# Optimization experiments

Measured on AMD Instinct MI355X. Metric: run time of the kernel, lower is better.

Reference implementation:

```python
import jax, jax.numpy as jnp
import numpy as np

B, U = 64, 512            # batch, max_units
AE = 1024
UE = 256                  # unit_embedding_size
A = 256                   # target_head_attention_size


def setup_inputs() -> dict:
    key = jax.random.key(0)
    ks = jax.random.split(key, 10)
    return {
        "autoregressive_embedding": jax.random.normal(ks[0], (B, U, AE), jnp.float32),
        "own_unit_embeddings": jax.random.normal(ks[1], (B, U, UE), jnp.float32),
        "enemy_unit_embeddings": jax.random.normal(ks[2], (B, U, UE), jnp.float32),
        "nr_own_units": jax.random.randint(ks[3], (B, 1), 0, U).astype(jnp.int64),
        "nr_units_enemy": jax.random.randint(ks[4], (B, 1), 0, U).astype(jnp.int64),
        "nr_own_flags": jax.random.randint(ks[5], (B, 1), 0, 8).astype(jnp.int64),
        "Wq": jax.random.normal(ks[6], (UE + AE, A), jnp.float32) * (1.0 / np.sqrt(UE + AE)),
        "bq": jnp.zeros((A,), jnp.float32),
        "Wk": jax.random.normal(ks[7], (UE, A), jnp.float32) * (1.0 / np.sqrt(UE)),
        "bk": jnp.zeros((A,), jnp.float32),
    }


def reference(autoregressive_embedding, own_unit_embeddings, enemy_unit_embeddings,
              nr_own_units, nr_units_enemy, nr_own_flags, Wq, bq, Wk, bk):
    # combined: [B, U, AE+UE]
    combined = jnp.concatenate([autoregressive_embedding, own_unit_embeddings], axis=2)
    queries = combined @ Wq + bq                       # [B, U, A]
    keys = enemy_unit_embeddings @ Wk + bk             # [B, U, A]
    attention = jnp.einsum("bqd,bkd->bqk", queries, keys) / (A ** 0.5)  # [B, U, U]
    # Vectorized mask: rows in [nr_own_flags, nr_own_units), cols in [0, nr_units_enemy)
    idx = jnp.arange(U)
    row_ok = (idx[None, :] >= nr_own_flags) & (idx[None, :] < nr_own_units)  # [B, U]
    col_ok = idx[None, :] < nr_units_enemy                                   # [B, U]
    mask = jnp.where(row_ok[:, :, None] & col_ok[:, None, :], 1.0, 1e-9)     # [B, U, U]
    return jax.nn.softmax(attention * mask, axis=-1)
```

## Files before the change

### kernel.cpp

```cpp
#include <hip/hip_runtime.h>

constexpr int B  = 64;
constexpr int U  = 512;
constexpr int AE = 1024;
constexpr int UE = 256;
constexpr int A  = 256;
constexpr int KQ = AE + UE;

typedef _Float16 f16x8 __attribute__((ext_vector_type(8)));
typedef float    f32x4 __attribute__((ext_vector_type(4)));


__global__ void prep(const float* __restrict__ Wq, const float* __restrict__ Wk,
                     _Float16* __restrict__ BTq, _Float16* __restrict__ BTk) {
    int idx = blockIdx.x * 256 + threadIdx.x;
    const float* W;
    _Float16* Dst;
    int rem;
    if (idx < 20 * 2 * 256 * 32) { W = Wq; Dst = BTq; rem = idx; }
    else                         { W = Wk; Dst = BTk; rem = idx - 20 * 2 * 256 * 32; }
    int pos = rem & 31;
    int row = (rem >> 5) & 255;
    int kp  = rem >> 13;
    int s = pos >> 3, e = pos & 7;
    int c = ((s ^ ((row >> 1) & 3)) << 3) | e;
    int k = kp * 32 + c;
    Dst[rem] = (_Float16)W[(size_t)k * 256 + row];
}

__global__ __launch_bounds__(512) void gemm(
    const float* __restrict__ A1, int s1, int split,
    const float* __restrict__ A2, int s2,
    const _Float16* __restrict__ BT,
    const float* __restrict__ bias,
    _Float16* __restrict__ Out,
    int Ktot)
{
    __shared__ __align__(16) _Float16 Al[2][2][64][32];
    __shared__ __align__(16) _Float16 Bl[2][2][256][32];

    const int t    = threadIdx.x;
    const int lane = t & 63;
    const int w    = t >> 6;
    const int mbase = blockIdx.x * 64;

    const int wm = (w & 1) * 32;
    const int wn = (w >> 1) * 64;

    f32x4 acc[2][4] = {};

    const int ar  = t >> 3;
    const int aq  = t & 7;
    const int ap  = aq >> 2;
    const int asw = ((aq & 3) ^ ((ar >> 1) & 3)) * 8;
    const size_t grow = mbase + ar;

    float4 areg0, areg1;

    auto loadA = [&](int k0) {
        int kg = k0 + aq * 8;
        const float* src = (kg < split) ? (A1 + grow * (size_t)s1 + kg)
                                        : (A2 + grow * (size_t)s2 + (kg - split));
        areg0 = ((const float4*)src)[0];
        areg1 = ((const float4*)src)[1];
    };
    auto stageB = [&](int kb, int nb) {
        const char* g = (const char*)BT + (size_t)kb * 32768 + w * 4096 + (lane << 4);
        char* l = (char*)(&Bl[nb][0][0][0]) + w * 4096;
        #pragma unroll
        for (int i = 0; i < 4; i++)
            __builtin_amdgcn_global_load_lds(
                (const __attribute__((address_space(1))) void*)(g + i * 1024),
                (__attribute__((address_space(3))) void*)(l + i * 1024), 16, 0, 0);
    };
    auto writeA = [&](int nb) {
        f16x8 hv;
        hv[0] = (_Float16)areg0.x; hv[1] = (_Float16)areg0.y;
        hv[2] = (_Float16)areg0.z; hv[3] = (_Float16)areg0.w;
        hv[4] = (_Float16)areg1.x; hv[5] = (_Float16)areg1.y;
        hv[6] = (_Float16)areg1.z; hv[7] = (_Float16)areg1.w;
        *(f16x8*)(&Al[nb][ap][ar][asw]) = hv;
    };

    loadA(0);
    stageB(0, 0);
    writeA(0);
    asm volatile("s_waitcnt vmcnt(0) lgkmcnt(0)" ::: "memory");
    __builtin_amdgcn_s_barrier();
    __builtin_amdgcn_sched_barrier(0);

    const int rsw = (((lane & 15) >> 1) & 3);
    const int nk = Ktot >> 6;
    int cur = 0;
    for (int kb = 0; kb < nk; kb++) {
        const bool more = (kb + 1 < nk);
        if (more) {
            loadA(kb * 64 + 64);
            stageB(kb + 1, cur ^ 1);
        }
        __builtin_amdgcn_sched_barrier(0);
        #pragma unroll
        for (int p = 0; p < 2; p++) {
            f16x8 af[2], bf[4];
            #pragma unroll
            for (int mt = 0; mt < 2; mt++)
                af[mt] = *(const f16x8*)(&Al[cur][p][wm + mt * 16 + (lane & 15)][(((lane >> 4) ^ rsw)) * 8]);
            #pragma unroll
            for (int nt = 0; nt < 4; nt++)
                bf[nt] = *(const f16x8*)(&Bl[cur][p][wn + nt * 16 + (lane & 15)][(((lane >> 4) ^ rsw)) * 8]);
            #pragma unroll
            for (int mt = 0; mt < 2; mt++)
                #pragma unroll
                for (int nt = 0; nt < 4; nt++)
                    acc[mt][nt] = __builtin_amdgcn_mfma_f32_16x16x32_f16(
                        af[mt], bf[nt], acc[mt][nt], 0, 0, 0);
        }
        __builtin_amdgcn_sched_barrier(0);
        if (more) writeA(cur ^ 1);
        asm volatile("s_waitcnt vmcnt(0) lgkmcnt(0)" ::: "memory");
        __builtin_amdgcn_s_barrier();
        __builtin_amdgcn_sched_barrier(0);
        cur ^= 1;
    }

    const int col0 = wn + (lane & 15);
    const int rsub = (lane >> 4) * 4;
    #pragma unroll
    for (int nt = 0; nt < 4; nt++) {
        const int col = col0 + nt * 16;
        const float bv = bias[col];
        const int c5 = col >> 5, c31 = col & 31;
        const int sc = c31 >> 3, ei = c31 & 7;
        #pragma unroll
        for (int mt = 0; mt < 2; mt++)
            #pragma unroll
            for (int r = 0; r < 4; r++) {
                int row = mbase + wm + mt * 16 + rsub + r;
                int bb = row >> 9, u = row & 511;
                int posb = ((sc ^ ((u >> 1) & 3)) << 3) | ei;
                Out[(((size_t)bb * 8 + c5) * 512 + u) * 32 + posb] =
                    (_Float16)(acc[mt][nt][r] + bv);
            }
    }
}

__global__ __launch_bounds__(512) void attn(
    const _Float16* __restrict__ Qh, const _Float16* __restrict__ Kh,
    const int* __restrict__ nr_own_units, const int* __restrict__ nr_units_enemy,
    const int* __restrict__ nr_own_flags, float* __restrict__ Out)
{
    __shared__ __align__(16) _Float16 Ql[8][64][32];
    __shared__ __align__(16) _Float16 Kl[512][32];
    __shared__ float red[64][4];

    const int t    = threadIdx.x;
    const int lane = t & 63;
    const int w    = t >> 6;
    const int b    = blockIdx.y;
    const int qbase = blockIdx.x * 64;

    const int nf = nr_own_flags[b];
    const int nu = nr_own_units[b];
    const int ne = nr_units_enemy[b];

    const int wm = (w & 1) * 32;
    const int wn = (w >> 1) * 128;

    f16x8 qreg[4];
    {
        const _Float16* Qb = Qh + ((size_t)b * 8 * 512 + qbase) * 32;
        #pragma unroll
        for (int j = 0; j < 4; j++) {
            int s = j * 512 + t;
            int p = s >> 8, row = (s & 255) >> 2, cq = s & 3;
            qreg[j] = *(const f16x8*)(Qb + ((size_t)p * 512 + row) * 32 + cq * 8);
        }
        #pragma unroll
        for (int j = 0; j < 4; j++) {
            int s = j * 512 + t;
            int p = s >> 8, row = (s & 255) >> 2, cq = s & 3;
            *(f16x8*)(&Ql[p][row][cq * 8]) = qreg[j];
        }
    }

    const _Float16* Kb = Kh + (size_t)b * 8 * 512 * 32;
    f16x8 kreg[4];
    const int krow = t >> 2;
    const int kq   = t & 3;
    auto loadK = [&](int c) {
        const _Float16* Kc = Kb + (size_t)c * 512 * 32;
        #pragma unroll
        for (int j = 0; j < 4; j++)
            kreg[j] = *(const f16x8*)(Kc + ((size_t)(j * 128 + krow)) * 32 + kq * 8);
    };
    loadK(0);

    f32x4 acc[2][8] = {};
    const int rsw = (((lane & 15) >> 1) & 3);
    for (int c = 0; c < 8; c++) {
        __syncthreads();
        #pragma unroll
        for (int j = 0; j < 4; j++) {
            int row = j * 128 + krow;
            *(f16x8*)(&Kl[row][kq * 8]) = kreg[j];
        }
        __syncthreads();
        if (c < 7) loadK(c + 1);
        f16x8 af[2], bf[8];
        #pragma unroll
        for (int mt = 0; mt < 2; mt++)
            af[mt] = *(const f16x8*)(&Ql[c][wm + mt * 16 + (lane & 15)][((lane >> 4) ^ rsw) * 8]);
        #pragma unroll
        for (int nt = 0; nt < 8; nt++)
            bf[nt] = *(const f16x8*)(&Kl[wn + nt * 16 + (lane & 15)][((lane >> 4) ^ rsw) * 8]);
        #pragma unroll
        for (int mt = 0; mt < 2; mt++)
            #pragma unroll
            for (int nt = 0; nt < 8; nt++)
                acc[mt][nt] = __builtin_amdgcn_mfma_f32_16x16x32_f16(
                    af[mt], bf[nt], acc[mt][nt], 0, 0, 0);
    }

    const int rsub = (lane >> 4) * 4;
    #pragma unroll
    for (int mt = 0; mt < 2; mt++)
        #pragma unroll
        for (int nt = 0; nt < 8; nt++)
            #pragma unroll
            for (int r = 0; r < 4; r++) {
                int rl = wm + mt * 16 + rsub + r;
                int uq = qbase + rl;
                int col = wn + nt * 16 + (lane & 15);
                bool ok = (col < ne) && (uq >= nf) && (uq < nu);
                acc[mt][nt][r] = acc[mt][nt][r] * 0.0625f * (ok ? 1.0f : 1e-9f);
            }

    float mx[2][4];
    #pragma unroll
    for (int mt = 0; mt < 2; mt++)
        #pragma unroll
        for (int r = 0; r < 4; r++) {
            float m = acc[mt][0][r];
            #pragma unroll
            for (int nt = 1; nt < 8; nt++) m = fmaxf(m, acc[mt][nt][r]);
            #pragma unroll
            for (int off = 1; off <= 8; off <<= 1) m = fmaxf(m, __shfl_xor(m, off));
            mx[mt][r] = m;
        }
    if ((lane & 15) == 0) {
        #pragma unroll
        for (int mt = 0; mt < 2; mt++)
            #pragma unroll
            for (int r = 0; r < 4; r++)
                red[wm + mt * 16 + rsub + r][w >> 1] = mx[mt][r];
    }
    __syncthreads();
    #pragma unroll
    for (int mt = 0; mt < 2; mt++)
        #pragma unroll
        for (int r = 0; r < 4; r++) {
            f32x4 v = *(const f32x4*)(&red[wm + mt * 16 + rsub + r][0]);
            mx[mt][r] = fmaxf(fmaxf(v[0], v[1]), fmaxf(v[2], v[3]));
        }
    __syncthreads();

    float sm[2][4];
    #pragma unroll
    for (int mt = 0; mt < 2; mt++)
        #pragma unroll
        for (int r = 0; r < 4; r++) {
            float s = 0.f;
            #pragma unroll
            for (int nt = 0; nt < 8; nt++) {
                float e = __expf(acc[mt][nt][r] - mx[mt][r]);
                acc[mt][nt][r] = e;
                s += e;
            }
            #pragma unroll
            for (int off = 1; off <= 8; off <<= 1) s += __shfl_xor(s, off);
            sm[mt][r] = s;
        }
    if ((lane & 15) == 0) {
        #pragma unroll
        for (int mt = 0; mt < 2; mt++)
            #pragma unroll
            for (int r = 0; r < 4; r++)
                red[wm + mt * 16 + rsub + r][w >> 1] = sm[mt][r];
    }
    __syncthreads();

    #pragma unroll
    for (int mt = 0; mt < 2; mt++)
        #pragma unroll
        for (int r = 0; r < 4; r++) {
            int rl = wm + mt * 16 + rsub + r;
            f32x4 v = *(const f32x4*)(&red[rl][0]);
            float inv = 1.0f / (v[0] + v[1] + v[2] + v[3]);
            float* orow = Out + ((size_t)b * 512 + qbase + rl) * 512 + wn + (lane & 15);
            #pragma unroll
            for (int nt = 0; nt < 8; nt++)
                orow[nt * 16] = acc[mt][nt][r] * inv;
        }
}

extern "C" void kernel_launch(void* const* d_in, const int* in_sizes, int n_in,
                              void* d_out, int out_size, void* d_ws, size_t ws_size,
                              hipStream_t stream) {
    const float* ar    = (const float*)d_in[0];
    const float* own   = (const float*)d_in[1];
    const float* enemy = (const float*)d_in[2];
    const int*   n_own   = (const int*)d_in[3];
    const int*   n_enemy = (const int*)d_in[4];
    const int*   n_flags = (const int*)d_in[5];
    const float* Wq = (const float*)d_in[6];
    const float* bq = (const float*)d_in[7];
    const float* Wk = (const float*)d_in[8];
    const float* bk = (const float*)d_in[9];
    float* out = (float*)d_out;

    char* ws = (char*)d_ws;
    _Float16* BTq = (_Float16*)(ws);
    _Float16* BTk = (_Float16*)(ws + 655360);
    _Float16* Qh  = (_Float16*)(ws + 786432);
    _Float16* Kh  = (_Float16*)(ws + 786432 + 16777216);

    prep<<<dim3(1536), dim3(256), 0, stream>>>(Wq, Wk, BTq, BTk);

    gemm<<<dim3(512), dim3(512), 0, stream>>>(ar, AE, AE, own, UE, BTq, bq, Qh, KQ);
    gemm<<<dim3(512), dim3(512), 0, stream>>>(enemy, UE, 0, enemy, UE, BTk, bk, Kh, A);

    attn<<<dim3(8, B), dim3(512), 0, stream>>>(Qh, Kh, n_own, n_enemy, n_flags, out);
}
```

Measured before the change: 322.6 us.

## Deepen projection GEMM pipeline to four LDS stages with K=32 steps

Restructures the projection GEMM main loop from a double-buffered K=64 step into a four-stage ring of K=32 slices. B tiles are prefetched three steps ahead and A two steps ahead, and the wait uses a partial vmcnt instead of draining all loads. This aims to hide global load latency behind MFMA work. In exchange it doubles the number of barriers per K and adds clamped redundant loads at the tail, and it relies on the vmcnt(5) count being exactly right.

```diff
diff --git a/kernel.cpp b/kernel.cpp
--- a/kernel.cpp
+++ b/kernel.cpp
@@ -8,6 +8,7 @@
 constexpr int KQ = AE + UE;
 
 typedef _Float16 f16x8 __attribute__((ext_vector_type(8)));
+typedef _Float16 f16x4 __attribute__((ext_vector_type(4)));
 typedef float    f32x4 __attribute__((ext_vector_type(4)));
 
 
@@ -17,8 +18,8 @@
     const float* W;
     _Float16* Dst;
     int rem;
-    if (idx < 20 * 2 * 256 * 32) { W = Wq; Dst = BTq; rem = idx; }
-    else                         { W = Wk; Dst = BTk; rem = idx - 20 * 2 * 256 * 32; }
+    if (idx < 40 * 256 * 32) { W = Wq; Dst = BTq; rem = idx; }
+    else                     { W = Wk; Dst = BTk; rem = idx - 40 * 256 * 32; }
     int pos = rem & 31;
     int row = (rem >> 5) & 255;
     int kp  = rem >> 13;
@@ -36,11 +37,12 @@
     _Float16* __restrict__ Out,
     int Ktot)
 {
-    __shared__ __align__(16) _Float16 Al[2][2][64][32];
-    __shared__ __align__(16) _Float16 Bl[2][2][256][32];
+    __shared__ __align__(16) _Float16 Al[4][64][32];
+    __shared__ __align__(16) _Float16 Bl[4][256][32];
 
     const int t    = threadIdx.x;
     const int lane = t & 63;
+    const int l15  = lane & 15;
     const int w    = t >> 6;
     const int mbase = blockIdx.x * 64;
 
@@ -49,81 +51,87 @@
 
     f32x4 acc[2][4] = {};
 
-    const int ar  = t >> 3;
-    const int aq  = t & 7;
-    const int ap  = aq >> 2;
-    const int asw = ((aq & 3) ^ ((ar >> 1) & 3)) * 8;
+    const int ar = t >> 3;
+    const int aq = t & 7;
     const size_t grow = mbase + ar;
-
-    float4 areg0, areg1;
-
-    auto loadA = [&](int k0) {
-        int kg = k0 + aq * 8;
+    const int nk = Ktot >> 5;
+
+    auto loadA = [&](int kb, float4& dst) {
+        int kk = kb < nk ? kb : nk - 1;
+        int kg = kk * 32 + aq * 4;
         const float* src = (kg < split) ? (A1 + grow * (size_t)s1 + kg)
                                         : (A2 + grow * (size_t)s2 + (kg - split));
-        areg0 = ((const float4*)src)[0];
-        areg1 = ((const float4*)src)[1];
+        dst = *(const float4*)src;
     };
     auto stageB = [&](int kb, int nb) {
-        const char* g = (const char*)BT + (size_t)kb * 32768 + w * 4096 + (lane << 4);
-        char* l = (char*)(&Bl[nb][0][0][0]) + w * 4096;
-        #pragma unroll
-        for (int i = 0; i < 4; i++)
-            __builtin_amdgcn_global_load_lds(
-                (const __attribute__((address_space(1))) void*)(g + i * 1024),
-                (__attribute__((address_space(3))) void*)(l + i * 1024), 16, 0, 0);
-    };
-    auto writeA = [&](int nb) {
-        f16x8 hv;
-        hv[0] = (_Float16)areg0.x; hv[1] = (_Float16)areg0.y;
-        hv[2] = (_Float16)areg0.z; hv[3] = (_Float16)areg0.w;
-        hv[4] = (_Float16)areg1.x; hv[5] = (_Float16)areg1.y;
-        hv[6] = (_Float16)areg1.z; hv[7] = (_Float16)areg1.w;
-        *(f16x8*)(&Al[nb][ap][ar][asw]) = hv;
-    };
-
-    loadA(0);
+        int kk = kb < nk ? kb : nk - 1;
+        const char* g = (const char*)BT + ((size_t)kk << 14) + (w << 10) + (lane << 4);
+        char* l = (char*)(&Bl[nb][0][0]) + (w << 10) + (lane << 4);
+        __builtin_amdgcn_global_load_lds(
+            (const __attribute__((address_space(1))) void*)g,
+            (__attribute__((address_space(3))) void*)l, 16, 0, 0);
+        __builtin_amdgcn_global_load_lds(
+            (const __attribute__((address_space(1))) void*)(g + 8192),
+            (__attribute__((address_space(3))) void*)(l + 8192), 16, 0, 0);
+    };
+    auto writeA = [&](int nb, const float4& v) {
+        f16x4 hv;
+        hv[0] = (_Float16)v.x; hv[1] = (_Float16)v.y;
+        hv[2] = (_Float16)v.z; hv[3] = (_Float16)v.w;
+        *(f16x4*)(&Al[nb][ar][((aq >> 1) ^ ((ar >> 1) & 3)) * 8 + (aq & 1) * 4]) = hv;
+    };
+    const int rp = ((lane >> 4) ^ ((l15 >> 1) & 3)) * 8;
+    auto mfmaStep = [&](int bc) {
+        f16x8 af[2], bf[4];
+        #pragma unroll
+        for (int mt = 0; mt < 2; mt++)
+            af[mt] = *(const f16x8*)(&Al[bc][wm + mt * 16 + l15][rp]);
+        #pragma unroll
+        for (int nt = 0; nt < 4; nt++)
+            bf[nt] = *(const f16x8*)(&Bl[bc][wn + nt * 16 + l15][rp]);
+        #pragma unroll
+        for (int mt = 0; mt < 2; mt++)
+            #pragma unroll
+            for (int nt = 0; nt < 4; nt++)
+                acc[mt][nt] = __builtin_amdgcn_mfma_f32_16x16x32_f16(
+                    af[mt], bf[nt], acc[mt][nt], 0, 0, 0);
+    };
+
+    float4 aP0, aP1;
+
+    loadA(0, aP0);
     stageB(0, 0);
-    writeA(0);
-    asm volatile("s_waitcnt vmcnt(0) lgkmcnt(0)" ::: "memory");
+    __builtin_amdgcn_sched_barrier(0);
+    stageB(1, 1);
+    loadA(1, aP1);
+    stageB(2, 2);
+    __builtin_amdgcn_sched_barrier(0);
+    writeA(0, aP0);
+    asm volatile("s_waitcnt vmcnt(5) lgkmcnt(0)" ::: "memory");
     __builtin_amdgcn_s_barrier();
     __builtin_amdgcn_sched_barrier(0);
 
-    const int rsw = (((lane & 15) >> 1) & 3);
-    const int nk = Ktot >> 6;
-    int cur = 0;
-    for (int kb = 0; kb < nk; kb++) {
-        const bool more = (kb + 1 < nk);
-        if (more) {
-            loadA(kb * 64 + 64);
-            stageB(kb + 1, cur ^ 1);
-        }
+    auto iter = [&](int k, int bc, int bn1, int bn3, float4& aDst, float4& aSrc) {
+        loadA(k + 2, aDst);
+        stageB(k + 3, bn3);
         __builtin_amdgcn_sched_barrier(0);
-        #pragma unroll
-        for (int p = 0; p < 2; p++) {
-            f16x8 af[2], bf[4];
-            #pragma unroll
-            for (int mt = 0; mt < 2; mt++)
-                af[mt] = *(const f16x8*)(&Al[cur][p][wm + mt * 16 + (lane & 15)][(((lane >> 4) ^ rsw)) * 8]);
-            #pragma unroll
-            for (int nt = 0; nt < 4; nt++)
-                bf[nt] = *(const f16x8*)(&Bl[cur][p][wn + nt * 16 + (lane & 15)][(((lane >> 4) ^ rsw)) * 8]);
-            #pragma unroll
-            for (int mt = 0; mt < 2; mt++)
-                #pragma unroll
-                for (int nt = 0; nt < 4; nt++)
-                    acc[mt][nt] = __builtin_amdgcn_mfma_f32_16x16x32_f16(
-                        af[mt], bf[nt], acc[mt][nt], 0, 0, 0);
-        }
+        mfmaStep(bc);
         __builtin_amdgcn_sched_barrier(0);
-        if (more) writeA(cur ^ 1);
-        asm volatile("s_waitcnt vmcnt(0) lgkmcnt(0)" ::: "memory");
+        writeA(bn1, aSrc);
+        asm volatile("s_waitcnt vmcnt(5) lgkmcnt(0)" ::: "memory");
         __builtin_amdgcn_s_barrier();
         __builtin_amdgcn_sched_barrier(0);
-        cur ^= 1;
-    }
-
-    const int col0 = wn + (lane & 15);
+    };
+
+    for (int k4 = 0; k4 < nk; k4 += 4) {
+        iter(k4 + 0, 0, 1, 3, aP0, aP1);
+        iter(k4 + 1, 1, 2, 0, aP1, aP0);
+        iter(k4 + 2, 2, 3, 1, aP0, aP1);
+        iter(k4 + 3, 3, 0, 2, aP1, aP0);
+    }
+    asm volatile("s_waitcnt vmcnt(0)" ::: "memory");
+
+    const int col0 = wn + l15;
     const int rsub = (lane >> 4) * 4;
     #pragma unroll
     for (int nt = 0; nt < 4; nt++) {
```

Result: no change. 328.4 us (+1.8%).
